# Performance work log

Hardware: AMD Instinct MI355X
Metric: run time of the kernel (lower is better)

Reference implementation:

```python
import jax, jax.numpy as jnp
import numpy as np

N = 100000
NEG_SLOPE = 0.2
EPS = 1e-16


def gat_conv(x, edge_index, W, att_src, att_dst, bias, concat):
    # x: [N, Fin]; W: [Fin, H*C]; att_*: [H, C]; edge_index: [2, E] (with self loops)
    H, C = att_src.shape
    src, dst = edge_index[0], edge_index[1]
    h = (x @ W).reshape(-1, H, C)                       # [N, H, C]
    a_src = (h * att_src).sum(-1)                       # [N, H]
    a_dst = (h * att_dst).sum(-1)                       # [N, H]
    e = a_src[src] + a_dst[dst]                         # [E, H]
    e = jnp.where(e >= 0, e, NEG_SLOPE * e)             # LeakyReLU(0.2)
    # segment softmax over destination-node neighborhoods
    m = jax.ops.segment_max(e, dst, num_segments=N)     # [N, H]
    ex = jnp.exp(e - m[dst])
    denom = jax.ops.segment_sum(ex, dst, num_segments=N)
    alpha = ex / (denom[dst] + EPS)                     # [E, H]
    msg = h[src] * alpha[:, :, None]                    # [E, H, C]
    out = jax.ops.segment_sum(msg, dst, num_segments=N)  # [N, H, C]
    out = out.reshape(N, H * C) if concat else out.mean(axis=1)
    return out + bias


def setup_inputs() -> dict:
    key = jax.random.key(0)
    ks = jax.random.split(key, 10)
    Fin, Ch, Co, Hh = 256, 32, 64, 4
    E = 1600000
    x = jax.random.normal(ks[0], (N, Fin), dtype=jnp.float32)
    edge_index = jax.random.randint(ks[1], (2, E), 0, N, dtype=jnp.int64)
    s1 = 1.0 / np.sqrt(Fin)
    s2 = 1.0 / np.sqrt(Hh * Ch)
    W1 = jax.random.normal(ks[2], (Fin, Hh * Ch), dtype=jnp.float32) * s1
    att_src1 = jax.random.normal(ks[3], (Hh, Ch), dtype=jnp.float32) * (1.0 / np.sqrt(Ch))
    att_dst1 = jax.random.normal(ks[4], (Hh, Ch), dtype=jnp.float32) * (1.0 / np.sqrt(Ch))
    b1 = jnp.zeros((Hh * Ch,), dtype=jnp.float32)
    W2 = jax.random.normal(ks[5], (Hh * Ch, Co), dtype=jnp.float32) * s2
    att_src2 = jax.random.normal(ks[6], (1, Co), dtype=jnp.float32) * (1.0 / np.sqrt(Co))
    att_dst2 = jax.random.normal(ks[7], (1, Co), dtype=jnp.float32) * (1.0 / np.sqrt(Co))
    b2 = jnp.zeros((Co,), dtype=jnp.float32)
    return {"x": x, "edge_index": edge_index,
            "W1": W1, "att_src1": att_src1, "att_dst1": att_dst1, "b1": b1,
            "W2": W2, "att_src2": att_src2, "att_dst2": att_dst2, "b2": b2}


def reference(x, edge_index, W1, att_src1, att_dst1, b1, W2, att_src2, att_dst2, b2):
    # add self-loops (PyG GATConv default add_self_loops=True)
    loops = jnp.arange(N, dtype=edge_index.dtype)
    ei = jnp.concatenate([edge_index, jnp.stack([loops, loops])], axis=1)
    h = gat_conv(x, ei, W1, att_src1, att_dst1, b1, concat=True)
    h = jax.nn.elu(h)
    out = gat_conv(h, ei, W2, att_src2, att_dst2, b2, concat=False)
    return out
```

## Files before the change

kernel.cpp:

```cpp
#include <hip/hip_runtime.h>
#include <math.h>

typedef unsigned short ushort_t;
typedef unsigned int uint_t;
typedef __attribute__((ext_vector_type(8))) short short8;
typedef __attribute__((ext_vector_type(4))) float fx4;

__device__ __forceinline__ float bf16_to_f32(ushort_t u) {
    union { uint_t i; float f; } c;
    c.i = ((uint_t)u) << 16;
    return c.f;
}
__device__ __forceinline__ ushort_t f32_to_bf16(float f) {
    union { float f; uint_t i; } c;
    c.f = f;
    const uint_t x = c.i;
    return (ushort_t)((x + 0x7fffu + ((x >> 16) & 1u)) >> 16);
}

__global__ void convT_kernel(const float* __restrict__ W,
                             ushort_t* __restrict__ WT, int k, int m) {
    const int idx = blockIdx.x * 256 + threadIdx.x;
    if (idx >= k * m) return;
    const int mm = idx / k;
    const int kk = idx % k;
    WT[idx] = f32_to_bf16(W[(size_t)kk * m + mm]);
}

template <int TILES, bool A_F32, int K>
__global__ __launch_bounds__(256) void gemm_lds_kernel(
    const void* __restrict__ Avoid, const ushort_t* __restrict__ BT,
    ushort_t* __restrict__ C, int n) {
    constexpr int M = TILES * 16;
    constexpr int CH = K / 8;
    constexpr int NC = K / 32;
    __shared__ ushort_t lds[M * K];
    const int tid = threadIdx.x;

#pragma unroll
    for (int i = 0; i < (M * CH + 255) / 256; ++i) {
        const int idx = tid + i * 256;
        if (idx < M * CH) {
            const int row = idx / CH;
            const int c = idx - row * CH;
            *(short8*)&lds[(size_t)(row * CH + (c ^ (row & 7))) * 8] =
                *(const short8*)(BT + (size_t)row * K + c * 8);
        }
    }
    __syncthreads();

    const int wave = tid >> 6;
    const int lane = tid & 63;
    const int l15 = lane & 15;
    const int quad = lane >> 4;
    const int rowbase = blockIdx.x * 128 + wave * 32;
    const int r0 = min(rowbase + l15, n - 1);
    const int r1 = min(rowbase + 16 + l15, n - 1);
    const size_t off0 = (size_t)r0 * K + quad * 8;
    const size_t off1 = (size_t)r1 * K + quad * 8;

    fx4 acc[2][TILES];
#pragma unroll
    for (int rp = 0; rp < 2; ++rp)
#pragma unroll
        for (int t = 0; t < TILES; ++t) acc[rp][t] = (fx4){0.f, 0.f, 0.f, 0.f};

    fx4 c0a, c0b, c1a, c1b, n0a, n0b, n1a, n1b;
    short8 cb0, cb1, nb0, nb1;

    if constexpr (A_F32) {
        const float* A = (const float*)Avoid;
        c0a = *(const fx4*)(A + off0);
        c0b = *(const fx4*)(A + off0 + 4);
        c1a = *(const fx4*)(A + off1);
        c1b = *(const fx4*)(A + off1 + 4);
    } else {
        const ushort_t* A = (const ushort_t*)Avoid;
        cb0 = *(const short8*)(A + off0);
        cb1 = *(const short8*)(A + off1);
    }

#pragma unroll
    for (int kc = 0; kc < NC; ++kc) {
        if (kc + 1 < NC) {
            const int kd = (kc + 1) * 32;
            if constexpr (A_F32) {
                const float* A = (const float*)Avoid;
                n0a = *(const fx4*)(A + off0 + kd);
                n0b = *(const fx4*)(A + off0 + kd + 4);
                n1a = *(const fx4*)(A + off1 + kd);
                n1b = *(const fx4*)(A + off1 + kd + 4);
            } else {
                const ushort_t* A = (const ushort_t*)Avoid;
                nb0 = *(const short8*)(A + off0 + kd);
                nb1 = *(const short8*)(A + off1 + kd);
            }
        }
        short8 bf[TILES];
#pragma unroll
        for (int t = 0; t < TILES; ++t) {
            const int brow = t * 16 + l15;
            const int c = kc * 4 + quad;
            bf[t] = *(const short8*)&lds[(size_t)(brow * CH +
                                                  (c ^ (brow & 7))) * 8];
        }
        short8 af0, af1;
        if constexpr (A_F32) {
            union { short8 v; ushort_t u[8]; } u0, u1;
#pragma unroll
            for (int j = 0; j < 4; ++j) {
                u0.u[j] = f32_to_bf16(c0a[j]);
                u0.u[4 + j] = f32_to_bf16(c0b[j]);
                u1.u[j] = f32_to_bf16(c1a[j]);
                u1.u[4 + j] = f32_to_bf16(c1b[j]);
            }
            af0 = u0.v;
            af1 = u1.v;
        } else {
            af0 = cb0;
            af1 = cb1;
        }
#pragma unroll
        for (int t = 0; t < TILES; ++t) {
            acc[0][t] = __builtin_amdgcn_mfma_f32_16x16x32_bf16(af0, bf[t],
                                                                acc[0][t],
                                                                0, 0, 0);
            acc[1][t] = __builtin_amdgcn_mfma_f32_16x16x32_bf16(af1, bf[t],
                                                                acc[1][t],
                                                                0, 0, 0);
        }
        if (kc + 1 < NC) {
            if constexpr (A_F32) {
                c0a = n0a; c0b = n0b; c1a = n1a; c1b = n1b;
            } else {
                cb0 = nb0; cb1 = nb1;
            }
        }
    }

#pragma unroll
    for (int rp = 0; rp < 2; ++rp) {
        const int crow0 = rowbase + rp * 16 + quad * 4;
#pragma unroll
        for (int t = 0; t < TILES; ++t) {
#pragma unroll
            for (int r = 0; r < 4; ++r) {
                const int rr = crow0 + r;
                if (rr < n)
                    C[(size_t)rr * M + t * 16 + l15] =
                        f32_to_bf16(acc[rp][t][r]);
            }
        }
    }
}

template <int H, int C>
__global__ void att_kernel(const ushort_t* __restrict__ h,
                           const float* __restrict__ att_s,
                           const float* __restrict__ att_d,
                           float* __restrict__ as_, float* __restrict__ ad_,
                           int n) {
    const int idx = blockIdx.x * blockDim.x + threadIdx.x;
    if (idx >= n * H) return;
    const int node = idx / H;
    const int hh = idx % H;
    const ushort_t* hp = h + (size_t)node * H * C + hh * C;
    float s0 = 0.f, s1 = 0.f;
#pragma unroll
    for (int c = 0; c < C; ++c) {
        const float v = bf16_to_f32(hp[c]);
        s0 += v * att_s[hh * C + c];
        s1 += v * att_d[hh * C + c];
    }
    as_[idx] = s0;
    ad_[idx] = s1;
}

__global__ __launch_bounds__(1024) void hist_kernel(const int* __restrict__ dst,
                                                    int* __restrict__ histG,
                                                    int e, int chunk, int NB,
                                                    int G) {
    __shared__ int hl[512];
    for (int b = threadIdx.x; b < NB; b += 1024) hl[b] = 0;
    __syncthreads();
    const int g = blockIdx.x;
    const int lo = g * chunk;
    const int hi = min(lo + chunk, e);
    for (int i = lo + threadIdx.x; i < hi; i += 1024)
        atomicAdd(&hl[dst[i] >> 8], 1);
    __syncthreads();
    for (int b = threadIdx.x; b < NB; b += 1024) histG[b * G + g] = hl[b];
}

__global__ __launch_bounds__(1024) void scan1_kernel(const int* __restrict__ in,
                                                     int* __restrict__ out,
                                                     int* __restrict__ sums,
                                                     int n) {
    __shared__ int s[1024];
    const int t = threadIdx.x;
    const int i = blockIdx.x * 1024 + t;
    const int v = (i < n) ? in[i] : 0;
    s[t] = v;
    __syncthreads();
    for (int d = 1; d < 1024; d <<= 1) {
        const int x = (t >= d) ? s[t - d] : 0;
        __syncthreads();
        s[t] += x;
        __syncthreads();
    }
    if (i < n) out[i] = s[t] - v;
    if (t == 1023) sums[blockIdx.x] = s[1023];
}

__global__ __launch_bounds__(128) void scan2_kernel(int* sums, int nb) {
    __shared__ int s[128];
    const int t = threadIdx.x;
    const int v = (t < nb) ? sums[t] : 0;
    s[t] = v;
    __syncthreads();
    for (int d = 1; d < 128; d <<= 1) {
        const int x = (t >= d) ? s[t - d] : 0;
        __syncthreads();
        s[t] += x;
        __syncthreads();
    }
    if (t < nb) sums[t] = s[t] - v;
}

__global__ __launch_bounds__(1024) void scan3_kernel(int* __restrict__ out,
                                                     const int* __restrict__ sums,
                                                     int n) {
    const int i = blockIdx.x * 1024 + threadIdx.x;
    if (i < n) out[i] += sums[blockIdx.x];
}

__global__ __launch_bounds__(1024) void bin_kernel(const int* __restrict__ src,
                                                   const int* __restrict__ dst,
                                                   const int* __restrict__ base,
                                                   int2* __restrict__ binned,
                                                   int e, int chunk, int NB,
                                                   int G) {
    __shared__ int cur[512];
    const int g = blockIdx.x;
    for (int b = threadIdx.x; b < NB; b += 1024) cur[b] = base[b * G + g];
    __syncthreads();
    const int lo = g * chunk;
    const int hi = min(lo + chunk, e);
    for (int i = lo + threadIdx.x; i < hi; i += 1024) {
        const int d = dst[i];
        const int p = atomicAdd(&cur[d >> 8], 1);
        binned[p] = make_int2(src[i], d);
    }
}

#define BUILD_CAP 6144
__global__ __launch_bounds__(256) void build_kernel(
    const int2* __restrict__ binned, const int* __restrict__ base,
    int* __restrict__ csr, int* __restrict__ deg, int* __restrict__ offs,
    int e, int n, int NB, int G) {
    __shared__ int2 ep[BUILD_CAP];
    __shared__ int degL[256];
    __shared__ int offL[256];
    __shared__ int curL[256];
    const int b = blockIdx.x;
    const int tid = threadIdx.x;
    const int start = base[b * G];
    const int end = (b == NB - 1) ? e : base[(b + 1) * G];
    const int cnt = end - start;
    const bool stage = (cnt <= BUILD_CAP);
    degL[tid] = 0;
    if (stage)
        for (int i = tid; i < cnt; i += 256) ep[i] = binned[start + i];
    __syncthreads();
    if (stage) {
        for (int i = tid; i < cnt; i += 256) atomicAdd(&degL[ep[i].y & 255], 1);
    } else {
        for (int i = tid; i < cnt; i += 256)
            atomicAdd(&degL[binned[start + i].y & 255], 1);
    }
    __syncthreads();
    const int v = degL[tid];
    offL[tid] = v;
    __syncthreads();
    for (int d = 1; d < 256; d <<= 1) {
        const int x = (tid >= d) ? offL[tid - d] : 0;
        __syncthreads();
        offL[tid] += x;
        __syncthreads();
    }
    const int excl = offL[tid] - v;
    curL[tid] = excl;
    const int node = (b << 8) + tid;
    if (node < n) {
        deg[node] = v;
        offs[node] = start + excl;
    }
    __syncthreads();
    if (stage) {
        for (int i = tid; i < cnt; i += 256) {
            const int p = atomicAdd(&curL[ep[i].y & 255], 1);
            csr[start + p] = ep[i].x;
        }
    } else {
        for (int i = tid; i < cnt; i += 256) {
            const int2 pr = binned[start + i];
            const int p = atomicAdd(&curL[pr.y & 255], 1);
            csr[start + p] = pr.x;
        }
    }
}

template <int H, int C, bool DO_ELU, bool OUT_BF16>
__global__ __launch_bounds__(64) void agg_kernel(
    const ushort_t* __restrict__ h, const float* __restrict__ a_src,
    const float* __restrict__ a_dst, const int* __restrict__ csr,
    const int* __restrict__ offs, const int* __restrict__ deg,
    const float* __restrict__ bias, void* __restrict__ outv, int n) {
    constexpr int HC = H * C;
    constexpr int R = HC / 64;
    constexpr int U = 8;
    const int dst = blockIdx.x;
    const int lane = threadIdx.x;
    const int start = offs[dst];
    const int d = deg[dst];
    const int myh = lane & (H - 1);
    const int ch0 = lane * R;
    const int hh = ch0 / C;
    const float advm = a_dst[dst * H + myh];
    float acc0 = 0.f, acc1 = 0.f;
    float L = 0.f;

    {
        float e = a_src[dst * H + myh] + advm;
        e = fmaxf(e, 0.2f * e);
        const float p = __expf(e);
        L += p;
        const float a = (H > 1) ? __shfl(p, hh) : p;
        const ushort_t* hp = h + (size_t)dst * HC + ch0;
        if (R == 2) {
            const uint_t v = *(const uint_t*)hp;
            acc0 += a * bf16_to_f32((ushort_t)(v & 0xffffu));
            acc1 += a * bf16_to_f32((ushort_t)(v >> 16));
        } else {
            acc0 += a * bf16_to_f32(hp[0]);
        }
    }

    int j = 0;
    for (; j + U <= d; j += U) {
        int s[U];
        float es[U];
        uint_t hv[U];
#pragma unroll
        for (int u = 0; u < U; ++u) s[u] = csr[start + j + u];
#pragma unroll
        for (int u = 0; u < U; ++u) es[u] = a_src[s[u] * H + myh];
#pragma unroll
        for (int u = 0; u < U; ++u) {
            const ushort_t* hp = h + (size_t)s[u] * HC + ch0;
            if (R == 2) hv[u] = *(const uint_t*)hp;
            else hv[u] = (uint_t)hp[0];
        }
#pragma unroll
        for (int u = 0; u < U; ++u) {
            float e = es[u] + advm;
            e = fmaxf(e, 0.2f * e);
            const float p = __expf(e);
            L += p;
            const float a = (H > 1) ? __shfl(p, hh) : p;
            if (R == 2) {
                acc0 += a * bf16_to_f32((ushort_t)(hv[u] & 0xffffu));
                acc1 += a * bf16_to_f32((ushort_t)(hv[u] >> 16));
            } else {
                acc0 += a * bf16_to_f32((ushort_t)hv[u]);
            }
        }
    }
    for (; j < d; ++j) {
        const int src = csr[start + j];
        float e = a_src[src * H + myh] + advm;
        e = fmaxf(e, 0.2f * e);
        const float p = __expf(e);
        L += p;
        const float a = (H > 1) ? __shfl(p, hh) : p;
        const ushort_t* hp = h + (size_t)src * HC + ch0;
        if (R == 2) {
            const uint_t v = *(const uint_t*)hp;
            acc0 += a * bf16_to_f32((ushort_t)(v & 0xffffu));
            acc1 += a * bf16_to_f32((ushort_t)(v >> 16));
        } else {
            acc0 += a * bf16_to_f32(hp[0]);
        }
    }

    const float Ld = (H > 1) ? __shfl(L, hh) : L;
    const float linv = 1.f / (Ld + 1e-16f);
    float r0 = acc0 * linv + bias[ch0];
    if (DO_ELU) r0 = (r0 > 0.f) ? r0 : (__expf(r0) - 1.f);
    if (R == 2) {
        float r1 = acc1 * linv + bias[ch0 + 1];
        if (DO_ELU) r1 = (r1 > 0.f) ? r1 : (__expf(r1) - 1.f);
        if (OUT_BF16) {
            const uint_t packed =
                (uint_t)f32_to_bf16(r0) | ((uint_t)f32_to_bf16(r1) << 16);
            *(uint_t*)((ushort_t*)outv + (size_t)dst * HC + ch0) = packed;
        } else {
            *(float2*)((float*)outv + (size_t)dst * HC + ch0) =
                make_float2(r0, r1);
        }
    } else {
        if (OUT_BF16)
            ((ushort_t*)outv)[(size_t)dst * HC + ch0] = f32_to_bf16(r0);
        else
            ((float*)outv)[(size_t)dst * HC + ch0] = r0;
    }
}

extern "C" void kernel_launch(void* const* d_in, const int* in_sizes, int n_in,
                              void* d_out, int out_size, void* d_ws,
                              size_t ws_size, hipStream_t stream) {
    const float* x = (const float*)d_in[0];
    const int* ei = (const int*)d_in[1];
    const float* W1 = (const float*)d_in[2];
    const float* att_s1 = (const float*)d_in[3];
    const float* att_d1 = (const float*)d_in[4];
    const float* b1 = (const float*)d_in[5];
    const float* W2 = (const float*)d_in[6];
    const float* att_s2 = (const float*)d_in[7];
    const float* att_d2 = (const float*)d_in[8];
    const float* b2 = (const float*)d_in[9];

    const int N = in_sizes[0] / 256;
    const int E = in_sizes[1] / 2;
    const int* srcp = ei;
    const int* dstp = ei + E;

    const int NB = (N + 255) >> 8;
    const int G = 128;
    const int NBG = NB * G;
    const int chunk = (E + G - 1) / G;
    const int nbs = (NBG + 1023) / 1024;

    float* as1 = (float*)d_ws;
    float* ad1 = as1 + (size_t)N * 4;
    float* as2 = ad1 + (size_t)N * 4;
    float* ad2 = as2 + N;
    int* histG = (int*)(ad2 + N);
    int* base = histG + NBG;
    int* sums = base + NBG;
    int* deg = sums + 128;
    int* offs = deg + N;
    int* csr = offs + N;
    int2* binned = (int2*)(csr + E);
    ushort_t* h1 = (ushort_t*)binned;
    ushort_t* h2 = h1 + (size_t)N * 128;
    ushort_t* h1p = h2 + (size_t)N * 64;
    ushort_t* W1T = h1p + (size_t)N * 128;
    ushort_t* W2T = W1T + 128 * 256;

    convT_kernel<<<(256 * 128 + 255) / 256, 256, 0, stream>>>(W1, W1T, 256, 128);
    convT_kernel<<<(128 * 64 + 255) / 256, 256, 0, stream>>>(W2, W2T, 128, 64);

    hist_kernel<<<G, 1024, 0, stream>>>(dstp, histG, E, chunk, NB, G);
    scan1_kernel<<<nbs, 1024, 0, stream>>>(histG, base, sums, NBG);
    scan2_kernel<<<1, 128, 0, stream>>>(sums, nbs);
    scan3_kernel<<<nbs, 1024, 0, stream>>>(base, sums, NBG);
    bin_kernel<<<G, 1024, 0, stream>>>(srcp, dstp, base, binned, E, chunk, NB,
                                       G);
    build_kernel<<<NB, 256, 0, stream>>>(binned, base, csr, deg, offs, E, N,
                                         NB, G);

    const int gblk = (N + 127) / 128;

    gemm_lds_kernel<8, true, 256><<<gblk, 256, 0, stream>>>(x, W1T, h1, N);
    att_kernel<4, 32><<<(N * 4 + 255) / 256, 256, 0, stream>>>(h1, att_s1,
                                                               att_d1, as1,
                                                               ad1, N);
    agg_kernel<4, 32, true, true><<<N, 64, 0, stream>>>(h1, as1, ad1, csr,
                                                        offs, deg, b1, h1p, N);

    gemm_lds_kernel<4, false, 128><<<gblk, 256, 0, stream>>>(h1p, W2T, h2, N);
    att_kernel<1, 64><<<(N + 255) / 256, 256, 0, stream>>>(h2, att_s2, att_d2,
                                                           as2, ad2, N);
    agg_kernel<1, 64, false, false><<<N, 64, 0, stream>>>(h2, as2, ad2, csr,
                                                          offs, deg, b2, d_out,
                                                          N);
}
```

Before: 420.3 us.

## Pack four destination nodes per block and double-buffer neighbor gathers in aggregation

```diff
diff --git a/kernel.cpp b/kernel.cpp
--- a/kernel.cpp
+++ b/kernel.cpp
@@ -310,8 +310,21 @@
     }
 }
 
+template <int H>
+__device__ __forceinline__ float head_sel(const float* __restrict__ a,
+                                          int node, int myh) {
+    if constexpr (H == 1) {
+        return a[node];
+    } else {
+        const fx4 v = *(const fx4*)(a + (size_t)node * H);
+        const float lo = (myh & 1) ? v[1] : v[0];
+        const float hi = (myh & 1) ? v[3] : v[2];
+        return (myh & 2) ? hi : lo;
+    }
+}
+
 template <int H, int C, bool DO_ELU, bool OUT_BF16>
-__global__ __launch_bounds__(64) void agg_kernel(
+__global__ __launch_bounds__(256) void agg_kernel(
     const ushort_t* __restrict__ h, const float* __restrict__ a_src,
     const float* __restrict__ a_dst, const int* __restrict__ csr,
     const int* __restrict__ offs, const int* __restrict__ deg,
@@ -319,19 +332,21 @@
     constexpr int HC = H * C;
     constexpr int R = HC / 64;
     constexpr int U = 8;
-    const int dst = blockIdx.x;
-    const int lane = threadIdx.x;
+    const int lane = threadIdx.x & 63;
+    const int wv = __builtin_amdgcn_readfirstlane((int)(threadIdx.x >> 6));
+    const int dst = blockIdx.x * 4 + wv;
+    if (dst >= n) return;
     const int start = offs[dst];
     const int d = deg[dst];
     const int myh = lane & (H - 1);
     const int ch0 = lane * R;
     const int hh = ch0 / C;
-    const float advm = a_dst[dst * H + myh];
+    const float advm = head_sel<H>(a_dst, dst, myh);
     float acc0 = 0.f, acc1 = 0.f;
     float L = 0.f;
 
     {
-        float e = a_src[dst * H + myh] + advm;
+        float e = head_sel<H>(a_src, dst, myh) + advm;
         e = fmaxf(e, 0.2f * e);
         const float p = __expf(e);
         L += p;
@@ -346,52 +361,53 @@
         }
     }
 
-    int j = 0;
-    for (; j + U <= d; j += U) {
-        int s[U];
-        float es[U];
-        uint_t hv[U];
-#pragma unroll
-        for (int u = 0; u < U; ++u) s[u] = csr[start + j + u];
-#pragma unroll
-        for (int u = 0; u < U; ++u) es[u] = a_src[s[u] * H + myh];
-#pragma unroll
-        for (int u = 0; u < U; ++u) {
-            const ushort_t* hp = h + (size_t)s[u] * HC + ch0;
-            if (R == 2) hv[u] = *(const uint_t*)hp;
-            else hv[u] = (uint_t)hp[0];
-        }
-#pragma unroll
-        for (int u = 0; u < U; ++u) {
-            float e = es[u] + advm;
-            e = fmaxf(e, 0.2f * e);
-            const float p = __expf(e);
-            L += p;
-            const float a = (H > 1) ? __shfl(p, hh) : p;
-            if (R == 2) {
-                acc0 += a * bf16_to_f32((ushort_t)(hv[u] & 0xffffu));
-                acc1 += a * bf16_to_f32((ushort_t)(hv[u] >> 16));
-            } else {
-                acc0 += a * bf16_to_f32((ushort_t)hv[u]);
-            }
-        }
-    }
-    for (; j < d; ++j) {
-        const int src = csr[start + j];
-        float e = a_src[src * H + myh] + advm;
-        e = fmaxf(e, 0.2f * e);
-        const float p = __expf(e);
-        L += p;
-        const float a = (H > 1) ? __shfl(p, hh) : p;
-        const ushort_t* hp = h + (size_t)src * HC + ch0;
-        if (R == 2) {
-            const uint_t v = *(const uint_t*)hp;
-            acc0 += a * bf16_to_f32((ushort_t)(v & 0xffffu));
-            acc1 += a * bf16_to_f32((ushort_t)(v >> 16));
-        } else {
-            acc0 += a * bf16_to_f32(hp[0]);
-        }
-    }
+    const int nc = (d + U - 1) / U;
+    const int dm1 = (d > 0) ? d - 1 : 0;
+
+#define STAGE(cc, pX, hX)                                                   \
+    {                                                                       \
+        int sv_[U];                                                         \
+        _Pragma("unroll") for (int u = 0; u < U; ++u)                       \
+            sv_[u] = csr[start + min((cc) * U + u, dm1)];                   \
+        _Pragma("unroll") for (int u = 0; u < U; ++u) {                     \
+            const ushort_t* hp_ = h + (size_t)sv_[u] * HC + ch0;            \
+            if (R == 2) hX[u] = *(const uint_t*)hp_;                        \
+            else hX[u] = (uint_t)(*hp_);                                    \
+        }                                                                   \
+        _Pragma("unroll") for (int u = 0; u < U; ++u) {                     \
+            float e_ = head_sel<H>(a_src, sv_[u], myh) + advm;              \
+            e_ = fmaxf(e_, 0.2f * e_);                                      \
+            const float p_ = __expf(e_);                                    \
+            pX[u] = ((cc) * U + u < d) ? p_ : 0.f;                          \
+        }                                                                   \
+    }
+
+#define ACCUM(pX, hX)                                                      \
+    _Pragma("unroll") for (int u = 0; u < U; ++u) {                        \
+        L += pX[u];                                                        \
+        const float a_ = (H > 1) ? __shfl(pX[u], hh) : pX[u];              \
+        if (R == 2) {                                                      \
+            acc0 += a_ * bf16_to_f32((ushort_t)(hX[u] & 0xffffu));         \
+            acc1 += a_ * bf16_to_f32((ushort_t)(hX[u] >> 16));             \
+        } else {                                                           \
+            acc0 += a_ * bf16_to_f32((ushort_t)hX[u]);                     \
+        }                                                                  \
+    }
+
+    float pA[U], pB[U];
+    uint_t hA[U], hB[U];
+    if (nc > 0) {
+        STAGE(0, pA, hA);
+        if (nc > 1) STAGE(1, pB, hB);
+        for (int c = 0; c < nc; c += 2) {
+            ACCUM(pA, hA);
+            if (c + 2 < nc) STAGE(c + 2, pA, hA);
+            if (c + 1 < nc) ACCUM(pB, hB);
+            if (c + 3 < nc) STAGE(c + 3, pB, hB);
+        }
+    }
+#undef STAGE
+#undef ACCUM
 
     const float Ld = (H > 1) ? __shfl(L, hh) : L;
     const float linv = 1.f / (Ld + 1e-16f);
@@ -471,18 +487,20 @@
                                          NB, G);
 
     const int gblk = (N + 127) / 128;
+    const int ablk = (N + 3) / 4;
 
     gemm_lds_kernel<8, true, 256><<<gblk, 256, 0, stream>>>(x, W1T, h1, N);
     att_kernel<4, 32><<<(N * 4 + 255) / 256, 256, 0, stream>>>(h1, att_s1,
                                                                att_d1, as1,
                                                                ad1, N);
-    agg_kernel<4, 32, true, true><<<N, 64, 0, stream>>>(h1, as1, ad1, csr,
-                                                        offs, deg, b1, h1p, N);
+    agg_kernel<4, 32, true, true><<<ablk, 256, 0, stream>>>(h1, as1, ad1, csr,
+                                                            offs, deg, b1,
+                                                            h1p, N);
 
     gemm_lds_kernel<4, false, 128><<<gblk, 256, 0, stream>>>(h1p, W2T, h2, N);
     att_kernel<1, 64><<<(N + 255) / 256, 256, 0, stream>>>(h2, att_s2, att_d2,
                                                            as2, ad2, N);
-    agg_kernel<1, 64, false, false><<<N, 64, 0, stream>>>(h2, as2, ad2, csr,
-                                                          offs, deg, b2, d_out,
-                                                          N);
-}
+    agg_kernel<1, 64, false, false><<<ablk, 256, 0, stream>>>(h2, as2, ad2,
+                                                              csr, offs, deg,
+                                                              b2, d_out, N);
+}
```

New measurement: 496.8 us. 1.18x slower.
